# Kernel tuning notes

Hardware: AMD Instinct MI355X
Metric: run time of the kernel (lower is better)

Reference implementation:

```python
import jax, jax.numpy as jnp
import numpy as np

CHANNELS = 256
NUM_HEADS = 4
GROUPS = 8
EPS = 1e-5


def setup_inputs() -> dict:
    key = jax.random.key(0)
    ks = jax.random.split(key, 5)
    C = CHANNELS
    x = jax.random.normal(ks[0], (2, C, 16, 16, 16), dtype=jnp.float32)
    # GroupNorm affine params
    norm_w = jnp.ones((C,), dtype=jnp.float32)
    norm_b = jnp.zeros((C,), dtype=jnp.float32)
    # 1x1x1 Conv3d weights collapsed to dense matrices [out, in]
    fan = 1.0 / np.sqrt(C)
    qkv_w = jax.random.uniform(ks[1], (3 * C, C), jnp.float32, -fan, fan)
    qkv_b = jax.random.uniform(ks[2], (3 * C,), jnp.float32, -fan, fan)
    proj_w = jax.random.uniform(ks[3], (C, C), jnp.float32, -fan, fan)
    proj_b = jax.random.uniform(ks[4], (C,), jnp.float32, -fan, fan)
    return {"x": x, "norm_w": norm_w, "norm_b": norm_b,
            "qkv_w": qkv_w, "qkv_b": qkv_b,
            "proj_w": proj_w, "proj_b": proj_b}


def _group_norm(x, w, b):
    B, C, D, H, W = x.shape
    xg = x.reshape(B, GROUPS, C // GROUPS, D, H, W)
    mean = xg.mean(axis=(2, 3, 4, 5), keepdims=True)
    var = xg.var(axis=(2, 3, 4, 5), keepdims=True)
    xn = (xg - mean) * jax.lax.rsqrt(var + EPS)
    xn = xn.reshape(B, C, D, H, W)
    return xn * w[None, :, None, None, None] + b[None, :, None, None, None]


def reference(x, norm_w, norm_b, qkv_w, qkv_b, proj_w, proj_b):
    B, C, D, H, W = x.shape
    N = D * H * W
    hd = C // NUM_HEADS
    h = _group_norm(x, norm_w, norm_b)
    # 1x1x1 conv == channel matmul: [B, 3C, N]
    hf = h.reshape(B, C, N)
    qkv = jnp.einsum('oc,bcn->bon', qkv_w, hf) + qkv_b[None, :, None]
    q, k, v = jnp.split(qkv, 3, axis=1)
    q = q.reshape(B, NUM_HEADS, hd, N)
    k = k.reshape(B, NUM_HEADS, hd, N)
    v = v.reshape(B, NUM_HEADS, hd, N)
    scale = hd ** (-0.5)
    attn = jax.nn.softmax(jnp.einsum('bhcn,bhcm->bhnm', q, k) * scale, axis=-1)
    o = jnp.einsum('bhnm,bhcm->bhcn', attn, v)  # [B, H, hd, N]
    o = o.reshape(B, C, N)
    o = jnp.einsum('oc,bcn->bon', proj_w, o) + proj_b[None, :, None]
    return x + o.reshape(B, C, D, H, W)
```

## Files before the change

kernel.cpp:

```cpp
#include <hip/hip_runtime.h>
#include <hip/hip_bf16.h>

#define BATCH 2
#define CH 256
#define NH 4
#define HD 64
#define NGROUP 8
#define CPG 32
#define NTOK 4096
#define EPSV 1e-5f
#define QSCALE 0.1803368801111204f
#define NSPLIT 4

typedef __attribute__((ext_vector_type(8))) short short8;
typedef __attribute__((ext_vector_type(4))) short s4bf;
typedef __attribute__((ext_vector_type(4))) float float4v;

__device__ __forceinline__ unsigned short f2bf(float f) {
    union { float f; unsigned u; } v; v.f = f;
    unsigned r = v.u + 0x7FFF + ((v.u >> 16) & 1);
    return (unsigned short)(r >> 16);
}
__device__ __forceinline__ unsigned short f2bf_fast(float f) {
    union { float f; unsigned u; } v; v.f = f;
    return (unsigned short)((v.u + 0x8000u) >> 16);
}
__device__ __forceinline__ float bf2f(unsigned short u) {
    union { unsigned u; float f; } v; v.u = ((unsigned)u) << 16;
    return v.f;
}
__device__ __forceinline__ unsigned pk2bf(float a, float b) {
#if __has_builtin(__builtin_amdgcn_cvt_pk_bf16_f32)
    typedef __attribute__((ext_vector_type(2))) __bf16 bf2v;
    bf2v p = __builtin_amdgcn_cvt_pk_bf16_f32(a, b);
    union { bf2v v; unsigned u; } c; c.v = p;
    return c.u;
#else
    return (unsigned)f2bf_fast(a) | ((unsigned)f2bf_fast(b) << 16);
#endif
}

#define GL2LDS(g, l) __builtin_amdgcn_global_load_lds( \
    (const __attribute__((address_space(1))) void*)(g), \
    (__attribute__((address_space(3))) void*)(l), 16, 0, 0)

__global__ void prep(const float* __restrict__ x,
                     const float* __restrict__ qkv_w, const float* __restrict__ qkv_b,
                     const float* __restrict__ proj_w,
                     float* __restrict__ psum, float* __restrict__ psq,
                     unsigned short* __restrict__ wq, float* __restrict__ bq,
                     unsigned short* __restrict__ wp) {
    int bx = blockIdx.x;
    int t = threadIdx.x;
    if (bx < 256) {
        int s = bx & 15, g = (bx >> 4) & 7, b = bx >> 7;
        const float* base = x + ((size_t)(b * CH + g * CPG)) * NTOK + (size_t)s * 8192;
        float sum = 0.f, sq = 0.f;
        const float4v* p4 = (const float4v*)base;
        for (int i = 0; i < 8; ++i) {
            float4v v = p4[t + i * 256];
            for (int j = 0; j < 4; ++j) { sum += v[j]; sq += v[j] * v[j]; }
        }
        for (int off = 32; off; off >>= 1) {
            sum += __shfl_down(sum, off, 64);
            sq  += __shfl_down(sq,  off, 64);
        }
        __shared__ float ls[8];
        int wave = t >> 6, lane = t & 63;
        if (lane == 0) { ls[wave * 2] = sum; ls[wave * 2 + 1] = sq; }
        __syncthreads();
        if (t == 0) {
            float S = 0.f, Q = 0.f;
            for (int w = 0; w < 4; ++w) { S += ls[w * 2]; Q += ls[w * 2 + 1]; }
            int idx = (b * NGROUP + g) * 16 + s;
            psum[idx] = S; psq[idx] = Q;
        }
    } else {
        int idx = (bx - 256) * 256 + t;
        int stride = 256 * 256;
        for (int i = idx; i < 3 * CH * CH; i += stride) {
            float f = qkv_w[i];
            if (i < CH * CH) f *= QSCALE;
            wq[i] = f2bf(f);
        }
        for (int i = idx; i < CH * CH; i += stride) wp[i] = f2bf(proj_w[i]);
        for (int i = idx; i < 3 * CH; i += stride) {
            float f = qkv_b[i];
            if (i < CH) f *= QSCALE;
            bq[i] = f;
        }
    }
}

__global__ void gn_norm(const float* __restrict__ x, const float* __restrict__ nw,
                        const float* __restrict__ nb_, const float* __restrict__ psum,
                        const float* __restrict__ psq, unsigned short* __restrict__ hT) {
    int t = threadIdx.x;
    int n = blockIdx.x * 64 + (t & 63);
    int g = blockIdx.y;
    int cb = g * 32 + (t >> 6) * 8;
    int b = blockIdx.z;
    float S = 0.f, Q = 0.f;
    for (int s = 0; s < 16; ++s) {
        S += psum[(b * NGROUP + g) * 16 + s];
        Q += psq[(b * NGROUP + g) * 16 + s];
    }
    const float M = (float)(CPG * NTOK);
    float mean = S / M;
    float inv  = rsqrtf(Q / M - mean * mean + EPSV);
    short8 h8;
    for (int j = 0; j < 8; ++j) {
        int c = cb + j;
        float w  = nw[c] * inv;
        float bb = nb_[c] - mean * w;
        float v = x[((size_t)(b * CH + c)) * NTOK + n];
        h8[j] = (short)f2bf(v * w + bb);
    }
    *(short8*)(hT + ((size_t)b * NTOK + n) * CH + cb) = h8;
}

__global__ __launch_bounds__(256) void qkv_gemm(const unsigned short* __restrict__ hT,
        const unsigned short* __restrict__ wq, const float* __restrict__ bq,
        unsigned short* __restrict__ qT, unsigned short* __restrict__ kT,
        unsigned short* __restrict__ vv) {
    int f = blockIdx.x + 64 * blockIdx.y + 768 * blockIdx.z;
    int xcd = f & 7, j = f >> 3;
    int ob = j % 12;
    int p  = xcd + 8 * (j / 12);
    int nb = p & 63;
    int b  = p >> 6;
    int t = threadIdx.x;
    int wave = t >> 6, lane = t & 63;
    int l15 = lane & 15, quad = lane >> 4;
    int o0 = ob * 64 + wave * 16;

    __shared__ __align__(16) unsigned short bt[64 * 264];

    short8 aW[8];
    {
        const unsigned short* wr = wq + (size_t)(o0 + l15) * CH + quad * 8;
        for (int kc = 0; kc < 8; ++kc) aW[kc] = *(const short8*)(wr + kc * 32);
    }
    for (int p2 = 0; p2 < 8; ++p2) {
        int slot = p2 * 256 + t;
        int r = slot >> 5, c = slot & 31;
        *(short8*)(bt + r * 264 + c * 8) =
            *(const short8*)(hT + ((size_t)b * NTOK + nb * 64 + r) * CH + c * 8);
    }
    __syncthreads();

    float4v acc[4];
    for (int nt = 0; nt < 4; ++nt) for (int r = 0; r < 4; ++r) acc[nt][r] = 0.f;
    for (int kc = 0; kc < 8; ++kc) {
        for (int nt = 0; nt < 4; ++nt) {
            short8 pb = *(const short8*)(bt + (nt * 16 + l15) * 264 + kc * 32 + quad * 8);
            acc[nt] = __builtin_amdgcn_mfma_f32_16x16x32_bf16(aW[kc], pb, acc[nt], 0, 0, 0);
        }
    }
    int seg = ob >> 2;
    for (int nt = 0; nt < 4; ++nt) {
        int n = nb * 64 + nt * 16 + l15;
        if (seg < 2) {
            int ob_ = o0 + quad * 4;
            int cch = ob_ & 255;
            int hh = cch >> 6, ci = cch & 63;
            s4bf pk;
            for (int r = 0; r < 4; ++r)
                pk[r] = (short)f2bf(acc[nt][r] + bq[ob_ + r]);
            unsigned short* dst = (seg == 0) ? qT : kT;
            *(s4bf*)(dst + (((size_t)b * NH + hh) * NTOK + n) * HD + ci) = pk;
        } else {
            for (int r = 0; r < 4; ++r) {
                int o = o0 + quad * 4 + r;
                float val = acc[nt][r] + bq[o];
                int cch = o & 255;
                int hh = cch >> 6, ci = cch & 63;
                vv[(((size_t)b * NH + hh) * HD + ci) * NTOK + n] = f2bf(val);
            }
        }
    }
}

__global__ __launch_bounds__(256, 4) void attn_kernel(const unsigned short* __restrict__ qT,
        const unsigned short* __restrict__ kT, const unsigned short* __restrict__ vv,
        unsigned short* __restrict__ opb, float* __restrict__ lpb) {
    int f = blockIdx.x + 32 * blockIdx.y + 128 * blockIdx.z;
    int xcd = f & 7, j = f >> 3;
    int nb = j >> 2;
    int g  = xcd + 8 * (j & 3);
    int h  = g & 3;
    int zb = g >> 2;
    int sp = zb & 3, b = zb >> 2;
    int t = threadIdx.x, wave = t >> 6, lane = t & 63;
    int l15 = lane & 15, quad = lane >> 4;
    int n0 = nb * 128 + wave * 32;
    int kv0 = sp * (NTOK / NSPLIT);

    unsigned short* opart = opb + (size_t)sp * ((size_t)BATCH * NTOK * CH);
    float* lpart = lpb + (size_t)sp * (BATCH * NH * NTOK);

    const unsigned short* qbh = qT + ((size_t)(b * NH + h)) * NTOK * HD;
    const unsigned short* kbh = kT + ((size_t)(b * NH + h)) * NTOK * HD;
    const unsigned short* vbh = vv + ((size_t)(b * NH + h)) * HD * NTOK;

    __shared__ __align__(16) unsigned short kbuf[2][64 * 64];
    __shared__ __align__(16) unsigned short vbuf[2][64 * 64];

    short8 aQ[2][2];
    for (int mt = 0; mt < 2; ++mt) {
        aQ[mt][0] = *(const short8*)(qbh + (size_t)(n0 + mt * 16 + l15) * HD + quad * 8);
        aQ[mt][1] = *(const short8*)(qbh + (size_t)(n0 + mt * 16 + l15) * HD + 32 + quad * 8);
    }

    float l_p[2] = {0.f, 0.f};
    float4v o_acc[2][4];
    for (int mt = 0; mt < 2; ++mt)
        for (int ct = 0; ct < 4; ++ct)
            for (int r = 0; r < 4; ++r) o_acc[mt][ct][r] = 0.f;
    const float4v ZERO = {0.f, 0.f, 0.f, 0.f};

    #define STAGE_TILE(kb_, vb_, ms_)                                                  \
        do {                                                                           \
            _Pragma("unroll")                                                          \
            for (int i = 0; i < 2; ++i) {                                              \
                int slot = (wave * 2 + i) * 64 + lane;                                 \
                int r = slot >> 3, c = slot & 7;                                       \
                GL2LDS(kbh + (size_t)((ms_) + r) * HD + ((c ^ (r & 7)) << 3),          \
                       (kb_) + (wave * 2 + i) * 512);                                  \
            }                                                                          \
            _Pragma("unroll")                                                          \
            for (int i = 0; i < 2; ++i) {                                              \
                int slot = (wave * 2 + i) * 64 + lane;                                 \
                int r = slot >> 3, c = slot & 7;                                       \
                GL2LDS(vbh + (size_t)r * NTOK + (ms_) + ((c ^ (r & 7)) << 3),          \
                       (vb_) + (wave * 2 + i) * 512);                                  \
            }                                                                          \
        } while (0)

    STAGE_TILE(kbuf[0], vbuf[0], kv0);
    int cur = 0;

    for (int ms = kv0; ms < kv0 + NTOK / NSPLIT; ms += 64) {
        asm volatile("s_waitcnt vmcnt(0)" ::: "memory");
        __syncthreads();
        if (ms + 64 < kv0 + NTOK / NSPLIT)
            STAGE_TILE(kbuf[cur ^ 1], vbuf[cur ^ 1], ms + 64);
        const unsigned short* kb = kbuf[cur];
        const unsigned short* vb = vbuf[cur];

        float4v s[2][4];
        __builtin_amdgcn_s_setprio(1);
#pragma unroll
        for (int nt = 0; nt < 4; ++nt) {
            int krow = nt * 16 + l15;
            int r7 = krow & 7;
            short8 ak0 = *(const short8*)(kb + krow * 64 + ((quad ^ r7) << 3));
            short8 ak1 = *(const short8*)(kb + krow * 64 + (((quad + 4) ^ r7) << 3));
#pragma unroll
            for (int mt = 0; mt < 2; ++mt) {
                float4v z = __builtin_amdgcn_mfma_f32_16x16x32_bf16(ak0, aQ[mt][0], ZERO, 0, 0, 0);
                z = __builtin_amdgcn_mfma_f32_16x16x32_bf16(ak1, aQ[mt][1], z, 0, 0, 0);
                s[mt][nt] = z;
            }
        }
        __builtin_amdgcn_s_setprio(0);
        s4bf aP[2][4];
#pragma unroll
        for (int mt = 0; mt < 2; ++mt) {
#pragma unroll
            for (int nt = 0; nt < 4; ++nt) {
                float e0 = __builtin_amdgcn_exp2f(s[mt][nt][0]);
                float e1 = __builtin_amdgcn_exp2f(s[mt][nt][1]);
                float e2 = __builtin_amdgcn_exp2f(s[mt][nt][2]);
                float e3 = __builtin_amdgcn_exp2f(s[mt][nt][3]);
                l_p[mt] += (e0 + e1) + (e2 + e3);
                union { s4bf v; unsigned u[2]; } c;
                c.u[0] = pk2bf(e0, e1);
                c.u[1] = pk2bf(e2, e3);
                aP[mt][nt] = c.v;
            }
        }
        __builtin_amdgcn_s_setprio(1);
#pragma unroll
        for (int ct = 0; ct < 4; ++ct) {
#pragma unroll
            for (int nt = 0; nt < 4; ++nt) {
                int vr = ct * 16 + l15;
                int c8 = nt * 2 + (quad >> 1);
                s4bf bv = *(const s4bf*)(vb + vr * 64 +
                                         ((c8 ^ (vr & 7)) << 3) + ((quad & 1) << 2));
#pragma unroll
                for (int mt = 0; mt < 2; ++mt)
                    o_acc[mt][ct] = __builtin_amdgcn_mfma_f32_16x16x16bf16_1k(aP[mt][nt], bv, o_acc[mt][ct], 0, 0, 0);
            }
        }
        __builtin_amdgcn_s_setprio(0);
        cur ^= 1;
    }
    for (int mt = 0; mt < 2; ++mt) {
        l_p[mt] += __shfl_xor(l_p[mt], 16, 64);
        l_p[mt] += __shfl_xor(l_p[mt], 32, 64);
    }
    for (int mt = 0; mt < 2; ++mt) {
        for (int ct = 0; ct < 4; ++ct) {
            for (int r = 0; r < 4; ++r) {
                int n = n0 + mt * 16 + quad * 4 + r;
                int cg = h * HD + ct * 16 + l15;
                opart[((size_t)b * NTOK + n) * CH + cg] = f2bf(o_acc[mt][ct][r]);
            }
        }
        if (lane < 16)
            lpart[((size_t)(b * NH + h)) * NTOK + n0 + mt * 16 + lane] = l_p[mt];
    }
}

__global__ __launch_bounds__(256) void proj_gemm(const unsigned short* __restrict__ opb,
        const float* __restrict__ lpb, const unsigned short* __restrict__ wp,
        const float* __restrict__ proj_b, const float* __restrict__ x,
        float* __restrict__ out) {
    int f = blockIdx.x + 64 * blockIdx.y + 256 * blockIdx.z;
    int xcd = f & 7, j = f >> 3;
    int cb = j & 3;
    int p  = xcd + 8 * (j >> 2);
    int nb = p & 63;
    int b  = p >> 6;
    int t = threadIdx.x, wave = t >> 6, lane = t & 63;
    int l15 = lane & 15, quad = lane >> 4;
    int c0 = cb * 64 + wave * 16;
    const size_t OP = (size_t)BATCH * NTOK * CH;
    const size_t LP = (size_t)BATCH * NH * NTOK;

    __shared__ __align__(16) unsigned short bt[64 * 264];
    __shared__ float rl[64 * 4];

    short8 aW[8];
    {
        const unsigned short* wr = wp + (size_t)(c0 + l15) * CH + quad * 8;
        for (int kc = 0; kc < 8; ++kc) aW[kc] = *(const short8*)(wr + kc * 32);
    }
    {
        int r = t >> 2, h = t & 3;
        size_t lidx = ((size_t)(b * NH + h)) * NTOK + nb * 64 + r;
        float ls = (lpb[lidx] + lpb[LP + lidx]) + (lpb[2 * LP + lidx] + lpb[3 * LP + lidx]);
        rl[r * 4 + h] = 1.0f / ls;
    }
    __syncthreads();
    for (int p2 = 0; p2 < 8; ++p2) {
        int slot = p2 * 256 + t;
        int r = slot >> 5, c = slot & 31;
        size_t base = ((size_t)b * NTOK + nb * 64 + r) * CH + c * 8;
        short8 o0 = *(const short8*)(opb + base);
        short8 o1 = *(const short8*)(opb + OP + base);
        short8 o2 = *(const short8*)(opb + 2 * OP + base);
        short8 o3 = *(const short8*)(opb + 3 * OP + base);
        float rinv = rl[r * 4 + (c >> 3)];
        short8 m;
        for (int jj = 0; jj < 8; ++jj) {
            float ff = (bf2f((unsigned short)o0[jj]) + bf2f((unsigned short)o1[jj]))
                     + (bf2f((unsigned short)o2[jj]) + bf2f((unsigned short)o3[jj]));
            m[jj] = (short)f2bf(ff * rinv);
        }
        *(short8*)(bt + r * 264 + c * 8) = m;
    }
    __syncthreads();

    float4v acc[4];
    for (int nt = 0; nt < 4; ++nt) for (int r = 0; r < 4; ++r) acc[nt][r] = 0.f;
    for (int kc = 0; kc < 8; ++kc) {
        for (int nt = 0; nt < 4; ++nt) {
            short8 pb = *(const short8*)(bt + (nt * 16 + l15) * 264 + kc * 32 + quad * 8);
            acc[nt] = __builtin_amdgcn_mfma_f32_16x16x32_bf16(aW[kc], pb, acc[nt], 0, 0, 0);
        }
    }
    for (int nt = 0; nt < 4; ++nt) {
        int n = nb * 64 + nt * 16 + l15;
        for (int r = 0; r < 4; ++r) {
            int cc = c0 + quad * 4 + r;
            size_t idx = ((size_t)(b * CH + cc)) * NTOK + n;
            out[idx] = acc[nt][r] + proj_b[cc] + x[idx];
        }
    }
}

extern "C" void kernel_launch(void* const* d_in, const int* in_sizes, int n_in,
                              void* d_out, int out_size, void* d_ws, size_t ws_size,
                              hipStream_t stream) {
    const float* x      = (const float*)d_in[0];
    const float* norm_w = (const float*)d_in[1];
    const float* norm_b = (const float*)d_in[2];
    const float* qkv_w  = (const float*)d_in[3];
    const float* qkv_b  = (const float*)d_in[4];
    const float* proj_w = (const float*)d_in[5];
    const float* proj_b = (const float*)d_in[6];
    float* out = (float*)d_out;

    char* ws = (char*)d_ws;
    float* psum  = (float*)ws;
    float* psq   = (float*)(ws + 1024);
    float* bqs   = (float*)(ws + 4096);
    unsigned short* wqb = (unsigned short*)(ws + 8192);
    unsigned short* wpb = (unsigned short*)(ws + 401408);
    float* lpb = (float*)(ws + 532480);
    const size_t MB4 = 4194304;
    unsigned short* hT  = (unsigned short*)(ws + 2097152);
    unsigned short* opb = hT;
    unsigned short* qT = (unsigned short*)(ws + 2097152 + 4 * MB4);
    unsigned short* kT = (unsigned short*)(ws + 2097152 + 5 * MB4);
    unsigned short* vv = (unsigned short*)(ws + 2097152 + 6 * MB4);

    prep<<<dim3(512), dim3(256), 0, stream>>>(x, qkv_w, qkv_b, proj_w, psum, psq, wqb, bqs, wpb);
    gn_norm<<<dim3(64, 8, BATCH), dim3(256), 0, stream>>>(x, norm_w, norm_b, psum, psq, hT);
    qkv_gemm<<<dim3(64, 12, BATCH), dim3(256), 0, stream>>>(hT, wqb, bqs, qT, kT, vv);
    attn_kernel<<<dim3(32, NH, BATCH * NSPLIT), dim3(256), 0, stream>>>(qT, kT, vv, opb, lpb);
    proj_gemm<<<dim3(64, 4, BATCH), dim3(256), 0, stream>>>(opb, lpb, wpb, proj_b, x, out);
}
```

Baseline: 146.9 us.

## Fuse GroupNorm apply into QKV GEMM and stage Q/K stores through LDS

Removes the separate gn_norm kernel and its bf16 hT intermediate. Each QKV GEMM block now computes per-channel scale and shift from the partial sums, reads fp32 x directly, normalizes it and packs it into LDS. Q/K outputs are first written to LDS and then stored as contiguous 16-byte rows instead of scattered 8-byte writes. The cost is that each x tile is re-read by all 12 output-block CTAs in fp32, twice the bytes of the old bf16 hT, and the strided x loads are only 4 bytes wide.

```diff
diff --git a/kernel.cpp b/kernel.cpp
--- a/kernel.cpp
+++ b/kernel.cpp
@@ -92,34 +92,9 @@
     }
 }
 
-__global__ void gn_norm(const float* __restrict__ x, const float* __restrict__ nw,
-                        const float* __restrict__ nb_, const float* __restrict__ psum,
-                        const float* __restrict__ psq, unsigned short* __restrict__ hT) {
-    int t = threadIdx.x;
-    int n = blockIdx.x * 64 + (t & 63);
-    int g = blockIdx.y;
-    int cb = g * 32 + (t >> 6) * 8;
-    int b = blockIdx.z;
-    float S = 0.f, Q = 0.f;
-    for (int s = 0; s < 16; ++s) {
-        S += psum[(b * NGROUP + g) * 16 + s];
-        Q += psq[(b * NGROUP + g) * 16 + s];
-    }
-    const float M = (float)(CPG * NTOK);
-    float mean = S / M;
-    float inv  = rsqrtf(Q / M - mean * mean + EPSV);
-    short8 h8;
-    for (int j = 0; j < 8; ++j) {
-        int c = cb + j;
-        float w  = nw[c] * inv;
-        float bb = nb_[c] - mean * w;
-        float v = x[((size_t)(b * CH + c)) * NTOK + n];
-        h8[j] = (short)f2bf(v * w + bb);
-    }
-    *(short8*)(hT + ((size_t)b * NTOK + n) * CH + cb) = h8;
-}
-
-__global__ __launch_bounds__(256) void qkv_gemm(const unsigned short* __restrict__ hT,
+__global__ __launch_bounds__(256) void qkv_gemm(const float* __restrict__ x,
+        const float* __restrict__ nw, const float* __restrict__ nb_,
+        const float* __restrict__ psum, const float* __restrict__ psq,
         const unsigned short* __restrict__ wq, const float* __restrict__ bq,
         unsigned short* __restrict__ qT, unsigned short* __restrict__ kT,
         unsigned short* __restrict__ vv) {
@@ -135,17 +110,45 @@
     int o0 = ob * 64 + wave * 16;
 
     __shared__ __align__(16) unsigned short bt[64 * 264];
+    __shared__ float wch[256], bch[256];
+
+    {
+        int c = t;
+        int gg = c >> 5;
+        float S = 0.f, Q = 0.f;
+        for (int s = 0; s < 16; ++s) {
+            S += psum[(b * NGROUP + gg) * 16 + s];
+            Q += psq[(b * NGROUP + gg) * 16 + s];
+        }
+        const float M = (float)(CPG * NTOK);
+        float mean = S / M;
+        float inv  = rsqrtf(Q / M - mean * mean + EPSV);
+        float w = nw[c] * inv;
+        wch[c] = w;
+        bch[c] = nb_[c] - mean * w;
+    }
 
     short8 aW[8];
     {
         const unsigned short* wr = wq + (size_t)(o0 + l15) * CH + quad * 8;
         for (int kc = 0; kc < 8; ++kc) aW[kc] = *(const short8*)(wr + kc * 32);
     }
-    for (int p2 = 0; p2 < 8; ++p2) {
-        int slot = p2 * 256 + t;
-        int r = slot >> 5, c = slot & 31;
-        *(short8*)(bt + r * 264 + c * 8) =
-            *(const short8*)(hT + ((size_t)b * NTOK + nb * 64 + r) * CH + c * 8);
+    __syncthreads();
+
+    {
+        int n = t & 63, jj = t >> 6;
+        const float* xb = x + (size_t)b * CH * NTOK + (size_t)nb * 64 + n;
+        for (int i = 0; i < 16; ++i) {
+            int c0 = i * 16 + jj * 4;
+            float h0 = xb[(size_t)(c0 + 0) * NTOK] * wch[c0 + 0] + bch[c0 + 0];
+            float h1 = xb[(size_t)(c0 + 1) * NTOK] * wch[c0 + 1] + bch[c0 + 1];
+            float h2 = xb[(size_t)(c0 + 2) * NTOK] * wch[c0 + 2] + bch[c0 + 2];
+            float h3 = xb[(size_t)(c0 + 3) * NTOK] * wch[c0 + 3] + bch[c0 + 3];
+            union { s4bf v; unsigned u[2]; } pk;
+            pk.u[0] = pk2bf(h0, h1);
+            pk.u[1] = pk2bf(h2, h3);
+            *(s4bf*)(bt + n * 264 + c0) = pk.v;
+        }
     }
     __syncthreads();
 
@@ -158,18 +161,29 @@
         }
     }
     int seg = ob >> 2;
-    for (int nt = 0; nt < 4; ++nt) {
-        int n = nb * 64 + nt * 16 + l15;
-        if (seg < 2) {
+    if (seg < 2) {
+        int hh = ob & 3;
+        unsigned short* dst = (seg == 0) ? qT : kT;
+        unsigned short* ot = bt;
+        __syncthreads();
+        for (int nt = 0; nt < 4; ++nt) {
             int ob_ = o0 + quad * 4;
-            int cch = ob_ & 255;
-            int hh = cch >> 6, ci = cch & 63;
             s4bf pk;
             for (int r = 0; r < 4; ++r)
                 pk[r] = (short)f2bf(acc[nt][r] + bq[ob_ + r]);
-            unsigned short* dst = (seg == 0) ? qT : kT;
-            *(s4bf*)(dst + (((size_t)b * NH + hh) * NTOK + n) * HD + ci) = pk;
-        } else {
+            int ci = wave * 16 + quad * 4;
+            *(s4bf*)(ot + (nt * 16 + l15) * 72 + ci) = pk;
+        }
+        __syncthreads();
+        for (int ii = 0; ii < 2; ++ii) {
+            int id2 = ii * 256 + t;
+            int n = id2 >> 3, c16 = id2 & 7;
+            short8 row = *(const short8*)(ot + n * 72 + c16 * 8);
+            *(short8*)(dst + (((size_t)b * NH + hh) * NTOK + (size_t)nb * 64 + n) * HD + c16 * 8) = row;
+        }
+    } else {
+        for (int nt = 0; nt < 4; ++nt) {
+            int n = nb * 64 + nt * 16 + l15;
             for (int r = 0; r < 4; ++r) {
                 int o = o0 + quad * 4 + r;
                 float val = acc[nt][r] + bq[o];
@@ -402,15 +416,14 @@
     unsigned short* wpb = (unsigned short*)(ws + 401408);
     float* lpb = (float*)(ws + 532480);
     const size_t MB4 = 4194304;
-    unsigned short* hT  = (unsigned short*)(ws + 2097152);
-    unsigned short* opb = hT;
+    unsigned short* opb = (unsigned short*)(ws + 2097152);
     unsigned short* qT = (unsigned short*)(ws + 2097152 + 4 * MB4);
     unsigned short* kT = (unsigned short*)(ws + 2097152 + 5 * MB4);
     unsigned short* vv = (unsigned short*)(ws + 2097152 + 6 * MB4);
 
     prep<<<dim3(512), dim3(256), 0, stream>>>(x, qkv_w, qkv_b, proj_w, psum, psq, wqb, bqs, wpb);
-    gn_norm<<<dim3(64, 8, BATCH), dim3(256), 0, stream>>>(x, norm_w, norm_b, psum, psq, hT);
-    qkv_gemm<<<dim3(64, 12, BATCH), dim3(256), 0, stream>>>(hT, wqb, bqs, qT, kT, vv);
+    qkv_gemm<<<dim3(64, 12, BATCH), dim3(256), 0, stream>>>(x, norm_w, norm_b, psum, psq,
+                                                            wqb, bqs, qT, kT, vv);
     attn_kernel<<<dim3(32, NH, BATCH * NSPLIT), dim3(256), 0, stream>>>(qT, kT, vv, opb, lpb);
     proj_gemm<<<dim3(64, 4, BATCH), dim3(256), 0, stream>>>(opb, lpb, wpb, proj_b, x, out);
 }
```

Result: no change. 147.4 us (+0.3%).
